# Kernel tuning notes

Measured on AMD Instinct MI355X. Metric: run time of the kernel, lower is better.

Reference implementation:

```python
import jax, jax.numpy as jnp
import numpy as np

# Instant-NGP multi-resolution hash grid constants (match init_kwargs)
L = 16            # num_levels
F = 2             # level_dim (features per level)
LOG2T = 19
T = 1 << LOG2T    # hashmap entries per level
BASE = 16.0       # base_resolution
SCALE = 1.3819061 # per_level_scale
HIDDEN = 64
N = 500_000
P1 = jnp.uint32(2654435761)  # NGP spatial hash primes (prime for dim0 is 1)
P2 = jnp.uint32(805459861)
# 8 corner offsets of the voxel, [8,3]
OFFS = jnp.array([[i, j, k] for i in (0, 1) for j in (0, 1) for k in (0, 1)], dtype=jnp.float32)


def hash_encode(x, table):
    # x: [N,3] in [0,1];  table: [L,T,F]
    res = jnp.floor(BASE * SCALE ** jnp.arange(L, dtype=jnp.float32))   # [L]
    pos = x[None] * (res[:, None, None] - 1.0)                          # [L,N,3]
    p0 = jnp.floor(pos)
    f = pos - p0                                                        # trilinear fracs [L,N,3]
    pi = p0.astype(jnp.uint32)                                          # [L,N,3]
    offs_u = OFFS.astype(jnp.uint32)                                    # [8,3]
    cx = pi[..., 0:1] + offs_u[None, None, :, 0]                        # [L,N,8]
    cy = pi[..., 1:2] + offs_u[None, None, :, 1]
    cz = pi[..., 2:3] + offs_u[None, None, :, 2]
    idx = (cx ^ (cy * P1) ^ (cz * P2)) & jnp.uint32(T - 1)              # [L,N,8] hashed table index
    feats = jax.vmap(lambda tab, i: tab[i])(table, idx)                 # per-level gather -> [L,N,8,F]
    # trilinear weights: prod over dims of (f if corner bit set else 1-f)
    w = jnp.prod(jnp.where(OFFS[None, None] > 0.5, f[:, :, None, :], 1.0 - f[:, :, None, :]), axis=-1)  # [L,N,8]
    out = jnp.einsum('lnc,lncf->lnf', w, feats)                         # [L,N,F]
    return out.transpose(1, 0, 2).reshape(x.shape[0], L * F)           # [N, L*F]


def setup_inputs() -> dict:
    key = jax.random.key(0)
    k = jax.random.split(key, 8)
    x = jax.random.uniform(k[0], (N, 3), dtype=jnp.float32)
    # NGP-style small uniform init for the hash tables
    table = jax.random.normal(k[1], (L, T, F), dtype=jnp.float32) * 1e-4
    feat_dim = L * F
    w1 = jax.random.normal(k[2], (feat_dim, HIDDEN), dtype=jnp.float32) / np.sqrt(feat_dim)
    b1 = jnp.zeros((HIDDEN,), jnp.float32)
    w2 = jax.random.normal(k[3], (HIDDEN, HIDDEN), dtype=jnp.float32) / np.sqrt(HIDDEN)
    b2 = jnp.zeros((HIDDEN,), jnp.float32)
    w3 = jax.random.normal(k[4], (HIDDEN, 3), dtype=jnp.float32) / np.sqrt(HIDDEN)
    b3 = jnp.zeros((3,), jnp.float32)
    return {"x": x, "table": table, "w1": w1, "b1": b1, "w2": w2, "b2": b2, "w3": w3, "b3": b3}


def reference(x, table, w1, b1, w2, b2, w3, b3):
    feat = hash_encode(x, table)                         # [N, 32]
    h = jax.nn.relu(feat @ w1 + b1)
    h = jax.nn.relu(h @ w2 + b2)
    rgb = jax.nn.sigmoid(h @ w3 + b3)                    # [N, 3]
    return rgb
```

## Files before the change

### kernel.cpp

```cpp
#include <hip/hip_runtime.h>
#include <hip/hip_fp16.h>
#include <math.h>


constexpr int      LVLS   = 16;
constexpr uint32_t TSIZE  = 1u << 19;
constexpr uint32_t TMASK  = TSIZE - 1u;
constexpr uint32_t PRIME1 = 2654435761u;
constexpr uint32_t PRIME2 = 805459861u;
constexpr float    SCALE_UP = 8192.f;
constexpr float    SCALE_DN = 1.f / 8192.f;

struct ResArr { float v[LVLS]; };

typedef __attribute__((ext_vector_type(8))) short short8v;
typedef __attribute__((ext_vector_type(4))) float float4v;
typedef __attribute__((ext_vector_type(2))) float float2v;

__device__ inline ushort f2bf(float f) {
    uint u = __float_as_uint(f);
    u += 0x7fffu + ((u >> 16) & 1u);
    return (ushort)(u >> 16);
}

__device__ inline uint pick4(const uint4& b, uint j) {
    const uint lo = (j & 1u) ? b.y : b.x;
    const uint hi = (j & 1u) ? b.w : b.z;
    return (j & 2u) ? hi : lo;
}

__global__ __launch_bounds__(256)
void ingp_pre(const float* __restrict__ table, uint* __restrict__ tab8,
              const float* __restrict__ x, float4* __restrict__ x4,
              const float* __restrict__ w1, const float* __restrict__ w2,
              const float* __restrict__ w3,
              ushort* __restrict__ w1t, ushort* __restrict__ w2t,
              ushort* __restrict__ w3t,
              int n, int bt_tab, int bt_x)
{
    const int b = blockIdx.x;
    if (b < bt_tab) {
        const int t = b * 256 + threadIdx.x;
        const float4 v = *reinterpret_cast<const float4*>(table + (size_t)t * 4u);
        const int lo = __builtin_amdgcn_cvt_pk_fp8_f32(v.x * SCALE_UP,
                                                       v.y * SCALE_UP, 0, false);
        const int hi = __builtin_amdgcn_cvt_pk_fp8_f32(v.z * SCALE_UP,
                                                       v.w * SCALE_UP, 0, false);
        tab8[t] = ((uint)lo & 0xffffu) | ((uint)hi << 16);
    } else if (b < bt_tab + bt_x) {
        const int i = (b - bt_tab) * 256 + threadIdx.x;
        if (i < n)
            x4[i] = make_float4(x[3 * i + 0], x[3 * i + 1], x[3 * i + 2], 0.f);
    } else {
        const int t = (b - bt_tab - bt_x) * 256 + threadIdx.x;
        if (t < 2048) {
            const int nn = t >> 5, k = t & 31;
            w1t[t] = f2bf(w1[k * 64 + nn]);
        } else if (t < 2048 + 4096) {
            const int q = t - 2048;
            const int nn = q >> 6, k = q & 63;
            w2t[q] = f2bf(w2[k * 64 + nn]);
        } else if (t < 2048 + 4096 + 1024) {
            const int q = t - 6144;
            const int nn = q >> 6, k = q & 63;
            w3t[q] = (nn < 3) ? f2bf(w3[k * 3 + nn]) : (ushort)0;
        }
    }
}

__global__ __launch_bounds__(256, 8)
void ingp_encode_f8(const float4* __restrict__ x4,
                    const ushort* __restrict__ tab8,
                    uint* __restrict__ feat, int n, ResArr res)
{
    const int i = blockIdx.x * 256 + threadIdx.x;
    const int l = blockIdx.y;
    if (i >= n) return;

    const float4 xp = x4[i];
    const float rm1 = res.v[l];
    const float px = xp.x * rm1, py = xp.y * rm1, pz = xp.z * rm1;
    const float fpx = floorf(px), fpy = floorf(py), fpz = floorf(pz);
    const float fx = px - fpx, fy = py - fpy, fz = pz - fpz;
    const uint32_t ix = (uint32_t)fpx;
    const uint32_t iy = (uint32_t)fpy;
    const uint32_t iz = (uint32_t)fpz;
    const uint32_t hy0 = iy * PRIME1, hy1 = (iy + 1u) * PRIME1;
    const uint32_t hz0 = iz * PRIME2, hz1 = (iz + 1u) * PRIME2;
    const ushort* tl = tab8 + (size_t)l * (size_t)TSIZE;

    uint32_t h0[4], h1[4];
    #pragma unroll
    for (int p = 0; p < 4; ++p) {
        const uint32_t bj = (p >> 1) & 1, bk = p & 1;
        const uint32_t hyz = (bj ? hy1 : hy0) ^ (bk ? hz1 : hz0);
        h0[p] = (ix ^ hyz) & TMASK;
        h1[p] = ((ix + 1u) ^ hyz) & TMASK;
    }

    const bool fast = (ix & 7u) != 7u;
    float2v c0v[4], c1v[4];
    #pragma unroll
    for (int p = 0; p < 4; ++p) {
        const uint32_t base = h0[p] & ~7u;
        const uint4 blk = *reinterpret_cast<const uint4*>(tl + base);
        const uint j0 = h0[p] & 7u;
        const uint w0 = pick4(blk, j0 >> 1) >> ((j0 & 1u) << 4);
        c0v[p] = __builtin_amdgcn_cvt_pk_f32_fp8((int)w0, false);
        const uint j1 = h1[p] & 7u;
        const uint w1e = pick4(blk, j1 >> 1) >> ((j1 & 1u) << 4);
        c1v[p] = __builtin_amdgcn_cvt_pk_f32_fp8((int)w1e, false);
    }
    if (!fast) {
        #pragma unroll
        for (int p = 0; p < 4; ++p)
            c1v[p] = __builtin_amdgcn_cvt_pk_f32_fp8((int)tl[h1[p]], false);
    }

    const float gx0 = (1.f - fx) * SCALE_DN, gx1 = fx * SCALE_DN;
    float a0 = 0.f, a1 = 0.f;
    #pragma unroll
    for (int p = 0; p < 4; ++p) {
        const int bj = (p >> 1) & 1, bk = p & 1;
        const float wyz = (bj ? fy : 1.f - fy) * (bk ? fz : 1.f - fz);
        const float w0 = wyz * gx0, w1 = wyz * gx1;
        a0 = fmaf(w0, c0v[p].x, a0);
        a1 = fmaf(w0, c0v[p].y, a1);
        a0 = fmaf(w1, c1v[p].x, a0);
        a1 = fmaf(w1, c1v[p].y, a1);
    }
    feat[(size_t)l * n + i] = (uint)f2bf(a0) | ((uint)f2bf(a1) << 16);
}

__global__ __launch_bounds__(256)
void ingp_mlp_mfma(const uint* __restrict__ feat,
                   const ushort* __restrict__ w1t,
                   const ushort* __restrict__ w2t,
                   const ushort* __restrict__ w3t,
                   const float* __restrict__ b1,
                   const float* __restrict__ b2,
                   const float* __restrict__ b3,
                   float* __restrict__ out, int n)
{
    __shared__ ushort s_h[4][64][72];
    const int tid = threadIdx.x;
    const int wv = tid >> 6;
    const int ln = tid & 63;
    const int lm = ln & 15;
    const int lk = ln >> 4;
    const int base = blockIdx.x * 256 + wv * 64;

    short8v a1[4];
    #pragma unroll
    for (int mt = 0; mt < 4; ++mt) {
        int pt = base + mt * 16 + lm;
        pt = pt < n ? pt : (n - 1);
        union { uint u[4]; short8v v; } c;
        #pragma unroll
        for (int j = 0; j < 4; ++j)
            c.u[j] = feat[(size_t)(lk * 4 + j) * (size_t)n + pt];
        a1[mt] = c.v;
    }

    float4v acc[4][4];
    #pragma unroll
    for (int nt = 0; nt < 4; ++nt) {
        const float bv = b1[nt * 16 + lm];
        #pragma unroll
        for (int mt = 0; mt < 4; ++mt)
            acc[mt][nt] = (float4v){bv, bv, bv, bv};
    }
    #pragma unroll
    for (int nt = 0; nt < 4; ++nt) {
        const short8v bfr = *(const short8v*)(w1t + (nt * 16 + lm) * 32 + lk * 8);
        #pragma unroll
        for (int mt = 0; mt < 4; ++mt)
            acc[mt][nt] = __builtin_amdgcn_mfma_f32_16x16x32_bf16(
                a1[mt], bfr, acc[mt][nt], 0, 0, 0);
    }
    #pragma unroll
    for (int mt = 0; mt < 4; ++mt)
        #pragma unroll
        for (int nt = 0; nt < 4; ++nt)
            #pragma unroll
            for (int r = 0; r < 4; ++r)
                s_h[wv][mt * 16 + lk * 4 + r][nt * 16 + lm] =
                    f2bf(fmaxf(acc[mt][nt][r], 0.f));
    __syncthreads();

    float4v acc2[4][4];
    #pragma unroll
    for (int nt = 0; nt < 4; ++nt) {
        const float bv = b2[nt * 16 + lm];
        #pragma unroll
        for (int mt = 0; mt < 4; ++mt)
            acc2[mt][nt] = (float4v){bv, bv, bv, bv};
    }
    #pragma unroll
    for (int ks = 0; ks < 2; ++ks) {
        short8v a2[4];
        #pragma unroll
        for (int mt = 0; mt < 4; ++mt)
            a2[mt] = *(const short8v*)&s_h[wv][mt * 16 + lm][ks * 32 + lk * 8];
        #pragma unroll
        for (int nt = 0; nt < 4; ++nt) {
            const short8v bfr =
                *(const short8v*)(w2t + (nt * 16 + lm) * 64 + ks * 32 + lk * 8);
            #pragma unroll
            for (int mt = 0; mt < 4; ++mt)
                acc2[mt][nt] = __builtin_amdgcn_mfma_f32_16x16x32_bf16(
                    a2[mt], bfr, acc2[mt][nt], 0, 0, 0);
        }
    }
    __syncthreads();
    #pragma unroll
    for (int mt = 0; mt < 4; ++mt)
        #pragma unroll
        for (int nt = 0; nt < 4; ++nt)
            #pragma unroll
            for (int r = 0; r < 4; ++r)
                s_h[wv][mt * 16 + lk * 4 + r][nt * 16 + lm] =
                    f2bf(fmaxf(acc2[mt][nt][r], 0.f));
    __syncthreads();

    float4v acc3[4];
    const float bv3 = (lm < 3) ? b3[lm] : 0.f;
    #pragma unroll
    for (int mt = 0; mt < 4; ++mt)
        acc3[mt] = (float4v){bv3, bv3, bv3, bv3};
    #pragma unroll
    for (int ks = 0; ks < 2; ++ks) {
        const short8v bfr = *(const short8v*)(w3t + lm * 64 + ks * 32 + lk * 8);
        #pragma unroll
        for (int mt = 0; mt < 4; ++mt) {
            const short8v a3 =
                *(const short8v*)&s_h[wv][mt * 16 + lm][ks * 32 + lk * 8];
            acc3[mt] = __builtin_amdgcn_mfma_f32_16x16x32_bf16(
                a3, bfr, acc3[mt], 0, 0, 0);
        }
    }
    if (lm < 3) {
        #pragma unroll
        for (int mt = 0; mt < 4; ++mt)
            #pragma unroll
            for (int r = 0; r < 4; ++r) {
                const int pt = base + mt * 16 + lk * 4 + r;
                if (pt < n)
                    out[pt * 3 + lm] = 1.f / (1.f + __expf(-acc3[mt][r]));
            }
    }
}

__global__ __launch_bounds__(256, 8)
void ingp_encode(const float* __restrict__ x,
                 const float* __restrict__ table,
                 uint* __restrict__ feat, int n, ResArr res)
{
    const int i = blockIdx.x * 256 + threadIdx.x;
    const int l = blockIdx.y;
    if (i >= n) return;
    const float xx = x[3 * i + 0], xy = x[3 * i + 1], xz = x[3 * i + 2];
    const float rm1 = res.v[l];
    const float px = xx * rm1, py = xy * rm1, pz = xz * rm1;
    const float fpx = floorf(px), fpy = floorf(py), fpz = floorf(pz);
    const float fx = px - fpx, fy = py - fpy, fz = pz - fpz;
    const uint32_t ix = (uint32_t)fpx, iy = (uint32_t)fpy, iz = (uint32_t)fpz;
    const uint32_t hy0 = iy * PRIME1, hy1 = (iy + 1u) * PRIME1;
    const uint32_t hz0 = iz * PRIME2, hz1 = (iz + 1u) * PRIME2;
    const float* tl = table + (size_t)l * (size_t)TSIZE * 2u;

    uint32_t idx0[4], idx1[4];
    #pragma unroll
    for (int p = 0; p < 4; ++p) {
        const uint32_t bj = (p >> 1) & 1, bk = p & 1;
        const uint32_t hyz = (bj ? hy1 : hy0) ^ (bk ? hz1 : hz0);
        idx0[p] = (ix ^ hyz) & TMASK;
        idx1[p] = ((ix + 1u) ^ hyz) & TMASK;
    }
    float2 c0[4], c1[4];
    if ((ix & 1u) == 0u) {
        #pragma unroll
        for (int p = 0; p < 4; ++p) {
            const uint32_t base = idx0[p] & ~1u;
            const float4 q = *reinterpret_cast<const float4*>(tl + (size_t)base * 2u);
            if (idx0[p] & 1u) { c0[p] = make_float2(q.z, q.w); c1[p] = make_float2(q.x, q.y); }
            else              { c0[p] = make_float2(q.x, q.y); c1[p] = make_float2(q.z, q.w); }
        }
    } else {
        #pragma unroll
        for (int p = 0; p < 4; ++p) {
            c0[p] = *reinterpret_cast<const float2*>(tl + (size_t)idx0[p] * 2u);
            c1[p] = *reinterpret_cast<const float2*>(tl + (size_t)idx1[p] * 2u);
        }
    }
    const float gx0 = 1.f - fx, gx1 = fx;
    float a0 = 0.f, a1 = 0.f;
    #pragma unroll
    for (int p = 0; p < 4; ++p) {
        const int bj = (p >> 1) & 1, bk = p & 1;
        const float wyz = (bj ? fy : 1.f - fy) * (bk ? fz : 1.f - fz);
        const float w0 = wyz * gx0, w1 = wyz * gx1;
        a0 = fmaf(w0, c0[p].x, a0);
        a1 = fmaf(w0, c0[p].y, a1);
        a0 = fmaf(w1, c1[p].x, a0);
        a1 = fmaf(w1, c1[p].y, a1);
    }
    feat[(size_t)l * n + i] = (uint)f2bf(a0) | ((uint)f2bf(a1) << 16);
}

__global__ __launch_bounds__(256)
void ingp_prep(const float* __restrict__ w1, const float* __restrict__ w2,
               const float* __restrict__ w3,
               ushort* __restrict__ w1t, ushort* __restrict__ w2t,
               ushort* __restrict__ w3t)
{
    const int t = blockIdx.x * 256 + threadIdx.x;
    if (t < 2048) {
        const int nn = t >> 5, k = t & 31;
        w1t[t] = f2bf(w1[k * 64 + nn]);
    } else if (t < 2048 + 4096) {
        const int q = t - 2048;
        const int nn = q >> 6, k = q & 63;
        w2t[q] = f2bf(w2[k * 64 + nn]);
    } else if (t < 2048 + 4096 + 1024) {
        const int q = t - 6144;
        const int nn = q >> 6, k = q & 63;
        w3t[q] = (nn < 3) ? f2bf(w3[k * 3 + nn]) : (ushort)0;
    }
}

extern "C" void kernel_launch(void* const* d_in, const int* in_sizes, int n_in,
                              void* d_out, int out_size, void* d_ws, size_t ws_size,
                              hipStream_t stream)
{
    const float* x     = (const float*)d_in[0];
    const float* table = (const float*)d_in[1];
    const float* w1    = (const float*)d_in[2];
    const float* b1    = (const float*)d_in[3];
    const float* w2    = (const float*)d_in[4];
    const float* b2    = (const float*)d_in[5];
    const float* w3    = (const float*)d_in[6];
    const float* b3    = (const float*)d_in[7];
    float* out = (float*)d_out;

    const int n = in_sizes[0] / 3;

    ResArr res;
    {
        const double S = (double)1.3819061f;
        double p = 1.0;
        for (int l = 0; l < LVLS; ++l) {
            res.v[l] = (float)floor(16.0 * p) - 1.0f;
            p *= S;
        }
    }

    const int gb = (n + 255) / 256;
    const size_t tab8_bytes = (size_t)LVLS * TSIZE * 2u;
    const size_t feat_bytes = (size_t)LVLS * (size_t)n * 4u;
    const size_t x4_bytes   = (size_t)n * 16u;

    const size_t off_tab8 = 32768;
    const size_t off_feat = off_tab8 + tab8_bytes;
    const size_t off_x4   = off_feat + feat_bytes;
    const size_t need_f8  = off_x4 + x4_bytes;
    const size_t need_mid = 16384 + feat_bytes;

    if (ws_size >= need_f8) {
        ushort* w1t  = (ushort*)d_ws;
        ushort* w2t  = w1t + 2048;
        ushort* w3t  = w2t + 4096;
        uint*   tab8 = (uint*)((char*)d_ws + off_tab8);
        uint*   feat = (uint*)((char*)d_ws + off_feat);
        float4* x4   = (float4*)((char*)d_ws + off_x4);

        const int bt_tab = (LVLS * (int)TSIZE / 2) / 256;
        const int bt_x   = gb;
        const int bt_w   = 28;
        ingp_pre<<<bt_tab + bt_x + bt_w, 256, 0, stream>>>(
            table, tab8, x, x4, w1, w2, w3, w1t, w2t, w3t, n, bt_tab, bt_x);

        dim3 gridA(gb, LVLS);
        ingp_encode_f8<<<gridA, 256, 0, stream>>>(x4, (const ushort*)tab8,
                                                  feat, n, res);
        ingp_mlp_mfma<<<gb, 256, 0, stream>>>(feat, w1t, w2t, w3t,
                                              b1, b2, b3, out, n);
    } else if (ws_size >= need_mid) {
        ushort* w1t = (ushort*)d_ws;
        ushort* w2t = w1t + 2048;
        ushort* w3t = w2t + 4096;
        uint*   feat = (uint*)((char*)d_ws + 16384);
        ingp_prep<<<28, 256, 0, stream>>>(w1, w2, w3, w1t, w2t, w3t);
        dim3 gridA(gb, LVLS);
        ingp_encode<<<gridA, 256, 0, stream>>>(x, table, feat, n, res);
        ingp_mlp_mfma<<<gb, 256, 0, stream>>>(feat, w1t, w2t, w3t,
                                              b1, b2, b3, out, n);
    }
}
```

Baseline: 178.6 us.

## Switch hash table cache from fp8 to fp16 and encode two points per thread

The pre-pass now converts the hash table to fp16 pairs (4 bytes per entry) instead of scaled fp8, which doubles the converted-table size and write traffic but drops the scale factors and fp8 conversion. The encode kernel now handles two points per thread, with 16-byte block loads that cover four entries, an xor-based neighbour test for the x+1 corner, and a paired 8-byte feature store. This aims to add memory-level parallelism per thread and halve the thread count. The costs are a larger table footprint in cache and a narrower fast-path window for reusing the loaded block.

Measured after the change: 209.7 us. +17.4%, slower.

```diff
diff --git a/kernel.cpp b/kernel.cpp
--- a/kernel.cpp
+++ b/kernel.cpp
@@ -8,14 +8,11 @@
 constexpr uint32_t TMASK  = TSIZE - 1u;
 constexpr uint32_t PRIME1 = 2654435761u;
 constexpr uint32_t PRIME2 = 805459861u;
-constexpr float    SCALE_UP = 8192.f;
-constexpr float    SCALE_DN = 1.f / 8192.f;
 
 struct ResArr { float v[LVLS]; };
 
 typedef __attribute__((ext_vector_type(8))) short short8v;
 typedef __attribute__((ext_vector_type(4))) float float4v;
-typedef __attribute__((ext_vector_type(2))) float float2v;
 
 __device__ inline ushort f2bf(float f) {
     uint u = __float_as_uint(f);
@@ -23,6 +20,11 @@
     return (ushort)(u >> 16);
 }
 
+__device__ inline float2 h2f(uint u) {
+    __half2 h = *reinterpret_cast<__half2*>(&u);
+    return __half22float2(h);
+}
+
 __device__ inline uint pick4(const uint4& b, uint j) {
     const uint lo = (j & 1u) ? b.y : b.x;
     const uint hi = (j & 1u) ? b.w : b.z;
@@ -30,7 +32,7 @@
 }
 
 __global__ __launch_bounds__(256)
-void ingp_pre(const float* __restrict__ table, uint* __restrict__ tab8,
+void ingp_pre(const float* __restrict__ table, uint* __restrict__ tab16,
               const float* __restrict__ x, float4* __restrict__ x4,
               const float* __restrict__ w1, const float* __restrict__ w2,
               const float* __restrict__ w3,
@@ -42,11 +44,12 @@
     if (b < bt_tab) {
         const int t = b * 256 + threadIdx.x;
         const float4 v = *reinterpret_cast<const float4*>(table + (size_t)t * 4u);
-        const int lo = __builtin_amdgcn_cvt_pk_fp8_f32(v.x * SCALE_UP,
-                                                       v.y * SCALE_UP, 0, false);
-        const int hi = __builtin_amdgcn_cvt_pk_fp8_f32(v.z * SCALE_UP,
-                                                       v.w * SCALE_UP, 0, false);
-        tab8[t] = ((uint)lo & 0xffffu) | ((uint)hi << 16);
+        __half2 ha = __floats2half2_rn(v.x, v.y);
+        __half2 hb = __floats2half2_rn(v.z, v.w);
+        uint2 o;
+        o.x = *reinterpret_cast<uint*>(&ha);
+        o.y = *reinterpret_cast<uint*>(&hb);
+        *reinterpret_cast<uint2*>(tab16 + (size_t)t * 2u) = o;
     } else if (b < bt_tab + bt_x) {
         const int i = (b - bt_tab) * 256 + threadIdx.x;
         if (i < n)
@@ -69,67 +72,88 @@
 }
 
 __global__ __launch_bounds__(256, 8)
-void ingp_encode_f8(const float4* __restrict__ x4,
-                    const ushort* __restrict__ tab8,
-                    uint* __restrict__ feat, int n, ResArr res)
-{
-    const int i = blockIdx.x * 256 + threadIdx.x;
+void ingp_encode2(const float4* __restrict__ x4,
+                  const uint* __restrict__ tab16,
+                  uint* __restrict__ feat, int n, ResArr res)
+{
+    const int i0 = (blockIdx.x * 256 + threadIdx.x) * 2;
     const int l = blockIdx.y;
-    if (i >= n) return;
-
-    const float4 xp = x4[i];
+    if (i0 >= n) return;
+    const bool two = (i0 + 1 < n);
+    const int i1 = two ? i0 + 1 : i0;
+
     const float rm1 = res.v[l];
-    const float px = xp.x * rm1, py = xp.y * rm1, pz = xp.z * rm1;
-    const float fpx = floorf(px), fpy = floorf(py), fpz = floorf(pz);
-    const float fx = px - fpx, fy = py - fpy, fz = pz - fpz;
-    const uint32_t ix = (uint32_t)fpx;
-    const uint32_t iy = (uint32_t)fpy;
-    const uint32_t iz = (uint32_t)fpz;
-    const uint32_t hy0 = iy * PRIME1, hy1 = (iy + 1u) * PRIME1;
-    const uint32_t hz0 = iz * PRIME2, hz1 = (iz + 1u) * PRIME2;
-    const ushort* tl = tab8 + (size_t)l * (size_t)TSIZE;
-
-    uint32_t h0[4], h1[4];
-    #pragma unroll
-    for (int p = 0; p < 4; ++p) {
-        const uint32_t bj = (p >> 1) & 1, bk = p & 1;
-        const uint32_t hyz = (bj ? hy1 : hy0) ^ (bk ? hz1 : hz0);
-        h0[p] = (ix ^ hyz) & TMASK;
-        h1[p] = ((ix + 1u) ^ hyz) & TMASK;
-    }
-
-    const bool fast = (ix & 7u) != 7u;
-    float2v c0v[4], c1v[4];
-    #pragma unroll
-    for (int p = 0; p < 4; ++p) {
-        const uint32_t base = h0[p] & ~7u;
-        const uint4 blk = *reinterpret_cast<const uint4*>(tl + base);
-        const uint j0 = h0[p] & 7u;
-        const uint w0 = pick4(blk, j0 >> 1) >> ((j0 & 1u) << 4);
-        c0v[p] = __builtin_amdgcn_cvt_pk_f32_fp8((int)w0, false);
-        const uint j1 = h1[p] & 7u;
-        const uint w1e = pick4(blk, j1 >> 1) >> ((j1 & 1u) << 4);
-        c1v[p] = __builtin_amdgcn_cvt_pk_f32_fp8((int)w1e, false);
-    }
-    if (!fast) {
+    const uint* tl = tab16 + (size_t)l * (size_t)TSIZE;
+
+    float fx[2], fy[2], fz[2];
+    uint h0[2][4], dx[2];
+    {
+        const float4 xa = x4[i0];
+        const float4 xb = x4[i1];
+        #pragma unroll
+        for (int q = 0; q < 2; ++q) {
+            const float4 xp = q ? xb : xa;
+            const float px = xp.x * rm1, py = xp.y * rm1, pz = xp.z * rm1;
+            const float fpx = floorf(px), fpy = floorf(py), fpz = floorf(pz);
+            fx[q] = px - fpx; fy[q] = py - fpy; fz[q] = pz - fpz;
+            const uint ix = (uint)fpx, iy = (uint)fpy, iz = (uint)fpz;
+            const uint hy0 = iy * PRIME1, hy1 = (iy + 1u) * PRIME1;
+            const uint hz0 = iz * PRIME2, hz1 = (iz + 1u) * PRIME2;
+            dx[q] = ix ^ (ix + 1u);
+            #pragma unroll
+            for (int p = 0; p < 4; ++p) {
+                const uint hyz = (((p >> 1) & 1) ? hy1 : hy0) ^
+                                 ((p & 1) ? hz1 : hz0);
+                h0[q][p] = (ix ^ hyz) & TMASK;
+            }
+        }
+    }
+
+    uint4 blk[2][4];
+    #pragma unroll
+    for (int q = 0; q < 2; ++q)
         #pragma unroll
         for (int p = 0; p < 4; ++p)
-            c1v[p] = __builtin_amdgcn_cvt_pk_f32_fp8((int)tl[h1[p]], false);
-    }
-
-    const float gx0 = (1.f - fx) * SCALE_DN, gx1 = fx * SCALE_DN;
-    float a0 = 0.f, a1 = 0.f;
-    #pragma unroll
-    for (int p = 0; p < 4; ++p) {
-        const int bj = (p >> 1) & 1, bk = p & 1;
-        const float wyz = (bj ? fy : 1.f - fy) * (bk ? fz : 1.f - fz);
-        const float w0 = wyz * gx0, w1 = wyz * gx1;
-        a0 = fmaf(w0, c0v[p].x, a0);
-        a1 = fmaf(w0, c0v[p].y, a1);
-        a0 = fmaf(w1, c1v[p].x, a0);
-        a1 = fmaf(w1, c1v[p].y, a1);
-    }
-    feat[(size_t)l * n + i] = (uint)f2bf(a0) | ((uint)f2bf(a1) << 16);
+            blk[q][p] = *reinterpret_cast<const uint4*>(tl + (h0[q][p] & ~3u));
+
+    uint fo[2];
+    #pragma unroll
+    for (int q = 0; q < 2; ++q) {
+        const bool fast = dx[q] <= 3u;
+        uint e0[4], e1[4];
+        #pragma unroll
+        for (int p = 0; p < 4; ++p) {
+            e0[p] = pick4(blk[q][p], h0[q][p] & 3u);
+            const uint h1v = h0[q][p] ^ dx[q];
+            e1[p] = fast ? pick4(blk[q][p], h1v & 3u) : 0u;
+        }
+        if (!fast) {
+            #pragma unroll
+            for (int p = 0; p < 4; ++p) e1[p] = tl[h0[q][p] ^ dx[q]];
+        }
+        const float gx0 = 1.f - fx[q], gx1 = fx[q];
+        float a0 = 0.f, a1 = 0.f;
+        #pragma unroll
+        for (int p = 0; p < 4; ++p) {
+            const float wyz = (((p >> 1) & 1) ? fy[q] : 1.f - fy[q]) *
+                              ((p & 1) ? fz[q] : 1.f - fz[q]);
+            const float w0 = wyz * gx0, w1 = wyz * gx1;
+            const float2 c0 = h2f(e0[p]);
+            const float2 c1 = h2f(e1[p]);
+            a0 = fmaf(w0, c0.x, a0);
+            a1 = fmaf(w0, c0.y, a1);
+            a0 = fmaf(w1, c1.x, a0);
+            a1 = fmaf(w1, c1.y, a1);
+        }
+        fo[q] = (uint)f2bf(a0) | ((uint)f2bf(a1) << 16);
+    }
+
+    if (two) {
+        uint2 o; o.x = fo[0]; o.y = fo[1];
+        *reinterpret_cast<uint2*>(feat + (size_t)l * n + i0) = o;
+    } else {
+        feat[(size_t)l * n + i0] = fo[0];
+    }
 }
 
 __global__ __launch_bounds__(256)
@@ -355,34 +379,34 @@
         }
     }
 
-    const int gb = (n + 255) / 256;
-    const size_t tab8_bytes = (size_t)LVLS * TSIZE * 2u;
-    const size_t feat_bytes = (size_t)LVLS * (size_t)n * 4u;
-    const size_t x4_bytes   = (size_t)n * 16u;
-
-    const size_t off_tab8 = 32768;
-    const size_t off_feat = off_tab8 + tab8_bytes;
-    const size_t off_x4   = off_feat + feat_bytes;
-    const size_t need_f8  = off_x4 + x4_bytes;
-    const size_t need_mid = 16384 + feat_bytes;
-
-    if (ws_size >= need_f8) {
-        ushort* w1t  = (ushort*)d_ws;
-        ushort* w2t  = w1t + 2048;
-        ushort* w3t  = w2t + 4096;
-        uint*   tab8 = (uint*)((char*)d_ws + off_tab8);
-        uint*   feat = (uint*)((char*)d_ws + off_feat);
-        float4* x4   = (float4*)((char*)d_ws + off_x4);
+    const int gb  = (n + 255) / 256;
+    const int gb2 = (n + 511) / 512;
+    const size_t tab16_bytes = (size_t)LVLS * TSIZE * 4u;
+    const size_t feat_bytes  = (size_t)LVLS * (size_t)n * 4u;
+    const size_t x4_bytes    = (size_t)n * 16u;
+
+    const size_t off_tab16 = 32768;
+    const size_t off_feat  = off_tab16 + tab16_bytes;
+    const size_t off_x4    = off_feat + feat_bytes;
+    const size_t need_full = off_x4 + x4_bytes;
+    const size_t need_mid  = 16384 + feat_bytes;
+
+    if (ws_size >= need_full) {
+        ushort* w1t   = (ushort*)d_ws;
+        ushort* w2t   = w1t + 2048;
+        ushort* w3t   = w2t + 4096;
+        uint*   tab16 = (uint*)((char*)d_ws + off_tab16);
+        uint*   feat  = (uint*)((char*)d_ws + off_feat);
+        float4* x4    = (float4*)((char*)d_ws + off_x4);
 
         const int bt_tab = (LVLS * (int)TSIZE / 2) / 256;
         const int bt_x   = gb;
         const int bt_w   = 28;
         ingp_pre<<<bt_tab + bt_x + bt_w, 256, 0, stream>>>(
-            table, tab8, x, x4, w1, w2, w3, w1t, w2t, w3t, n, bt_tab, bt_x);
-
-        dim3 gridA(gb, LVLS);
-        ingp_encode_f8<<<gridA, 256, 0, stream>>>(x4, (const ushort*)tab8,
-                                                  feat, n, res);
+            table, tab16, x, x4, w1, w2, w3, w1t, w2t, w3t, n, bt_tab, bt_x);
+
+        dim3 gridA(gb2, LVLS);
+        ingp_encode2<<<gridA, 256, 0, stream>>>(x4, tab16, feat, n, res);
         ingp_mlp_mfma<<<gb, 256, 0, stream>>>(feat, w1t, w2t, w3t,
                                               b1, b2, b3, out, n);
     } else if (ws_size >= need_mid) {
```
